# Optimization experiments

Measured on AMD Instinct MI355X. Metric: run time of the kernel, lower is better.

The kernel has to match this reference:

```python
import jax, jax.numpy as jnp
import numpy as np

N_NODES = 50000
N_EDGES = 800000
F_IN = 128
HEADS = 8
C = 16  # per-head channels (out_channels 128 // heads 8)
NEG_SLOPE = 0.2


def setup_inputs() -> dict:
    key = jax.random.key(0)
    k1, k2, k3, k4, k5, k6 = jax.random.split(key, 6)
    x = jax.random.normal(k1, (N_NODES, F_IN), dtype=jnp.float32)
    edge_index = jax.random.randint(k2, (2, N_EDGES), 0, N_NODES, dtype=jnp.int32)
    s = 1.0 / np.sqrt(F_IN)
    W_l = jax.random.normal(k3, (HEADS * C, F_IN), dtype=jnp.float32) * s
    W_r = jax.random.normal(k4, (HEADS * C, F_IN), dtype=jnp.float32) * s
    att = jax.random.normal(k5, (HEADS, C), dtype=jnp.float32) * s
    bias = jax.random.normal(k6, (HEADS * C,), dtype=jnp.float32) * 0.01
    return {"x": x, "edge_index": edge_index, "W_l": W_l, "W_r": W_r,
            "att": att, "bias": bias}


def reference(x, edge_index, W_l, W_r, att, bias):
    n = x.shape[0]
    src, dst = edge_index[0], edge_index[1]
    # node-level linear projections, reshaped to [n, H, C]
    x_l = (x @ W_l.T).reshape(n, HEADS, C)  # source features (x_j)
    x_r = (x @ W_r.T).reshape(n, HEADS, C)  # target features (x_i)
    x_j = x_l[src]          # [m, H, C] gathered per edge
    x_i = x_r[dst]          # [m, H, C]
    e = jax.nn.leaky_relu(x_i + x_j, NEG_SLOPE)      # [m, H, C]
    alpha = jnp.einsum('mhc,hc->mh', e, att)         # [m, H]
    # segment softmax over incoming edges of each target node (stable)
    amax = jax.ops.segment_max(alpha, dst, num_segments=n)   # [n, H]
    ea = jnp.exp(alpha - amax[dst])
    denom = jax.ops.segment_sum(ea, dst, num_segments=n)     # [n, H]
    alpha = ea / (denom[dst] + 1e-16)
    # scatter-aggregate messages x_j * alpha to target nodes
    out = jax.ops.segment_sum(x_j * alpha[..., None], dst, num_segments=n)
    out = out.reshape(n, HEADS * C) + bias  # concat heads + bias
    return out
```

## Files before the change

kernel.cpp:

```cpp
#include <hip/hip_runtime.h>
#include <hip/hip_fp16.h>
#include <math.h>


#define NN 50000
#define NE 800000
#define NHEADS 8
#define CH 16
#define FDIM 128
#define NEG_SLOPE 0.2f

#define BSHIFT 8
#define NBUCK ((NN + 255) >> 8)
#define BCAP 5120
#define CHUNK 4096
#define NCHUNK ((NE + CHUNK - 1) / CHUNK)

typedef _Float16 half8 __attribute__((ext_vector_type(8)));
typedef _Float16 h2v  __attribute__((ext_vector_type(2)));
typedef float f32x4 __attribute__((ext_vector_type(4)));

#define PBM 64
#define PTILES ((NN + PBM - 1) / PBM)

__global__ __launch_bounds__(512) void gat_proj_mfma(
        const float* __restrict__ x,
        const float* __restrict__ Wl,
        const float* __restrict__ Wr,
        __half* __restrict__ xl,
        __half* __restrict__ xr) {
    __shared__ __half Al[PBM][FDIM];
    __shared__ __half Bl[256][FDIM];

    const int t    = threadIdx.x;
    const int lane = t & 63;
    const int wave = t >> 6;
    const int wm   = wave >> 2;
    const int wn   = wave & 3;
    const int lr   = lane & 15;
    const int lh   = lane >> 4;

    const int row0 = blockIdx.x * PBM;

    #pragma unroll
    for (int i = 0; i < 2; ++i) {
        int c   = t + i * 512;
        int row = c >> 4;
        int c16 = c & 15;
        int sc  = c16 ^ (row & 7);
        int arow = row0 + row;
        if (arow >= NN) arow = NN - 1;
        const float4* src = reinterpret_cast<const float4*>(
            x + (size_t)arow * FDIM + c16 * 8);
        float4 v0 = src[0];
        float4 v1 = src[1];
        union { uint4 u; __half2 h[4]; } pk;
        pk.h[0] = __floats2half2_rn(v0.x, v0.y);
        pk.h[1] = __floats2half2_rn(v0.z, v0.w);
        pk.h[2] = __floats2half2_rn(v1.x, v1.y);
        pk.h[3] = __floats2half2_rn(v1.z, v1.w);
        *reinterpret_cast<uint4*>(&Al[row][sc * 8]) = pk.u;
    }
    #pragma unroll
    for (int i = 0; i < 8; ++i) {
        int c   = t + i * 512;
        int row = c >> 4;
        int c16 = c & 15;
        int sc  = c16 ^ (row & 7);
        const float* wr = (row < 128) ? (Wl + (size_t)row * FDIM)
                                      : (Wr + (size_t)(row - 128) * FDIM);
        const float4* src = reinterpret_cast<const float4*>(wr + c16 * 8);
        float4 v0 = src[0];
        float4 v1 = src[1];
        union { uint4 u; __half2 h[4]; } pk;
        pk.h[0] = __floats2half2_rn(v0.x, v0.y);
        pk.h[1] = __floats2half2_rn(v0.z, v0.w);
        pk.h[2] = __floats2half2_rn(v1.x, v1.y);
        pk.h[3] = __floats2half2_rn(v1.z, v1.w);
        *reinterpret_cast<uint4*>(&Bl[row][sc * 8]) = pk.u;
    }
    __syncthreads();

    f32x4 acc[2][4] = {};
    const char* Ab = reinterpret_cast<const char*>(&Al[0][0]);
    const char* Bb = reinterpret_cast<const char*>(&Bl[0][0]);

    #pragma unroll
    for (int kc = 0; kc < 4; ++kc) {
        half8 a[2], b[4];
        #pragma unroll
        for (int mi = 0; mi < 2; ++mi) {
            int row = wm * 32 + mi * 16 + lr;
            int bc  = (kc * 64 + 16 * lh) ^ ((row & 7) << 4);
            a[mi] = *reinterpret_cast<const half8*>(Ab + row * 256 + bc);
        }
        #pragma unroll
        for (int ni = 0; ni < 4; ++ni) {
            int row = wn * 64 + ni * 16 + lr;
            int bc  = (kc * 64 + 16 * lh) ^ ((row & 7) << 4);
            b[ni] = *reinterpret_cast<const half8*>(Bb + row * 256 + bc);
        }
        #pragma unroll
        for (int mi = 0; mi < 2; ++mi)
            #pragma unroll
            for (int ni = 0; ni < 4; ++ni)
                acc[mi][ni] = __builtin_amdgcn_mfma_f32_16x16x32_f16(
                    a[mi], b[ni], acc[mi][ni], 0, 0, 0);
    }

    #pragma unroll
    for (int mi = 0; mi < 2; ++mi) {
        #pragma unroll
        for (int ni = 0; ni < 4; ++ni) {
            int gc = wn * 64 + ni * 16 + lr;
            __half* outp = (gc < 128) ? xl : xr;
            int col = gc & 127;
            #pragma unroll
            for (int r = 0; r < 4; ++r) {
                int grow = row0 + wm * 32 + mi * 16 + 4 * lh + r;
                if (grow < NN)
                    outp[(size_t)grow * FDIM + col] = __float2half(acc[mi][ni][r]);
            }
        }
    }
}

__global__ void gat_init_cursor(int* __restrict__ bcursor) {
    int t = threadIdx.x;
    if (t < NBUCK) bcursor[t] = t * BCAP;
}

__global__ __launch_bounds__(256) void gat_bin_pass(
        const int* __restrict__ ei,
        int* __restrict__ bcursor,
        int2* __restrict__ binned) {
    __shared__ int hist[NBUCK];
    __shared__ int base_l[NBUCK];
    int t = threadIdx.x;
    for (int i = t; i < NBUCK; i += 256) hist[i] = 0;
    __syncthreads();

    int cbase = blockIdx.x * CHUNK;
    int s[CHUNK / 256], d[CHUNK / 256], r[CHUNK / 256];
    #pragma unroll
    for (int i = 0; i < CHUNK / 256; ++i) {
        int m = cbase + i * 256 + t;
        if (m < NE) {
            s[i] = ei[m];
            d[i] = ei[NE + m];
            r[i] = atomicAdd(&hist[d[i] >> BSHIFT], 1);
        } else {
            d[i] = -1;
        }
    }
    __syncthreads();
    for (int i = t; i < NBUCK; i += 256)
        base_l[i] = hist[i] ? atomicAdd(&bcursor[i], hist[i]) : 0;
    __syncthreads();
    #pragma unroll
    for (int i = 0; i < CHUNK / 256; ++i) {
        if (d[i] >= 0) {
            int pos = base_l[d[i] >> BSHIFT] + r[i];
            binned[pos] = make_int2(s[i], d[i] & 255);
        }
    }
}

__global__ __launch_bounds__(256) void gat_fine_pass(
        const int2* __restrict__ binned,
        const int* __restrict__ bcursor,
        int* __restrict__ rowstart,
        int* __restrict__ rowend,
        int* __restrict__ csr_src) {
    __shared__ int cnt_c[256];
    __shared__ int sbuf[256];
    __shared__ int cur_c[256];
    int t = threadIdx.x;
    int b = blockIdx.x;
    int base = b * BCAP;
    int cnt  = bcursor[b] - base;

    cnt_c[t] = 0;
    __syncthreads();
    for (int j = t; j < cnt; j += 256)
        atomicAdd(&cnt_c[binned[base + j].y], 1);
    __syncthreads();

    int v = cnt_c[t];
    sbuf[t] = v;
    __syncthreads();
    for (int off = 1; off < 256; off <<= 1) {
        int add = (t >= off) ? sbuf[t - off] : 0;
        __syncthreads();
        sbuf[t] += add;
        __syncthreads();
    }
    int excl = sbuf[t] - v;
    cur_c[t] = excl;
    int node = (b << BSHIFT) + t;
    if (node < NN) {
        rowstart[node] = base + excl;
        rowend[node]   = base + excl + v;
    }
    __syncthreads();

    for (int j = t; j < cnt; j += 256) {
        int2 e = binned[base + j];
        int pos = atomicAdd(&cur_c[e.y], 1);
        csr_src[base + pos] = e.x;
    }
}

__device__ __forceinline__ float gat_dot4_h(h2v e01, h2v e23,
                                            h2v at01, h2v at23) {
#if __has_builtin(__builtin_amdgcn_fdot2)
    float p = __builtin_amdgcn_fdot2(e01, at01, 0.0f, false);
    return __builtin_amdgcn_fdot2(e23, at23, p, false);
#else
    return (float)e01[0] * (float)at01[0] + (float)e01[1] * (float)at01[1]
         + (float)e23[0] * (float)at23[0] + (float)e23[1] * (float)at23[1];
#endif
}

__device__ __forceinline__ void gat_edge_step_h(
        const h2v xi01, const h2v xi23,
        const h2v at01, const h2v at23,
        uint2 raw, float4& acc, float& den) {
    union uh { unsigned u; h2v v; };
    uh j01, j23;
    j01.u = raw.x; j23.u = raw.y;
    h2v s01 = xi01 + j01.v;
    h2v s23 = xi23 + j23.v;
    uh b01, b23, a01, a23;
    b01.v = s01; b23.v = s23;
    a01.u = b01.u & 0x7FFF7FFFu;
    a23.u = b23.u & 0x7FFF7FFFu;
    const h2v c1 = {(_Float16)0.6f, (_Float16)0.6f};
    const h2v c2 = {(_Float16)0.4f, (_Float16)0.4f};
    h2v e01 = s01 * c1 + a01.v * c2;
    h2v e23 = s23 * c1 + a23.v * c2;
    float p = gat_dot4_h(e01, e23, at01, at23);
    p += __shfl_xor(p, 1);
    p += __shfl_xor(p, 2);
    float ea = __expf(p);
    acc.x = fmaf((float)j01.v[0], ea, acc.x);
    acc.y = fmaf((float)j01.v[1], ea, acc.y);
    acc.z = fmaf((float)j23.v[0], ea, acc.z);
    acc.w = fmaf((float)j23.v[1], ea, acc.w);
    den += ea;
}

__global__ __launch_bounds__(256) void gat_aggregate_kernel(
        const __half* __restrict__ xl,
        const __half* __restrict__ xr,
        const float* __restrict__ att,
        const float* __restrict__ bias,
        const int* __restrict__ rowstart,
        const int* __restrict__ rowend,
        const int* __restrict__ csr_src,
        float* __restrict__ out) {
    int node = blockIdx.x * 8 + (threadIdx.x >> 5);
    int u = threadIdx.x & 31;
    if (node >= NN) return;

    union { uint2 r; struct { unsigned a, b; } w; } xiraw;
    xiraw.r = *reinterpret_cast<const uint2*>(xr + (size_t)node * FDIM + u * 4);
    union uh { unsigned u; h2v v; };
    uh xi0, xi1;
    xi0.u = xiraw.w.a; xi1.u = xiraw.w.b;
    const float4 atf = *reinterpret_cast<const float4*>(att + u * 4);
    h2v a01 = {(_Float16)atf.x, (_Float16)atf.y};
    h2v a23 = {(_Float16)atf.z, (_Float16)atf.w};
    const float4 bi = *reinterpret_cast<const float4*>(bias + u * 4);
    int e0 = rowstart[node];
    int e1 = rowend[node];

    float4 acc0 = {0,0,0,0}, acc1 = {0,0,0,0}, acc2 = {0,0,0,0}, acc3 = {0,0,0,0};
    float den0 = 0.0f, den1 = 0.0f, den2 = 0.0f, den3 = 0.0f;

    int e = e0;
    for (; e + 4 <= e1; e += 4) {
        int s0 = csr_src[e + 0];
        int s1 = csr_src[e + 1];
        int s2 = csr_src[e + 2];
        int s3 = csr_src[e + 3];
        uint2 r0 = *reinterpret_cast<const uint2*>(xl + (size_t)s0 * FDIM + u * 4);
        uint2 r1 = *reinterpret_cast<const uint2*>(xl + (size_t)s1 * FDIM + u * 4);
        uint2 r2 = *reinterpret_cast<const uint2*>(xl + (size_t)s2 * FDIM + u * 4);
        uint2 r3 = *reinterpret_cast<const uint2*>(xl + (size_t)s3 * FDIM + u * 4);
        gat_edge_step_h(xi0.v, xi1.v, a01, a23, r0, acc0, den0);
        gat_edge_step_h(xi0.v, xi1.v, a01, a23, r1, acc1, den1);
        gat_edge_step_h(xi0.v, xi1.v, a01, a23, r2, acc2, den2);
        gat_edge_step_h(xi0.v, xi1.v, a01, a23, r3, acc3, den3);
    }
    for (; e < e1; ++e) {
        int s0 = csr_src[e];
        uint2 r0 = *reinterpret_cast<const uint2*>(xl + (size_t)s0 * FDIM + u * 4);
        gat_edge_step_h(xi0.v, xi1.v, a01, a23, r0, acc0, den0);
    }

    float4 acc;
    acc.x = (acc0.x + acc1.x) + (acc2.x + acc3.x);
    acc.y = (acc0.y + acc1.y) + (acc2.y + acc3.y);
    acc.z = (acc0.z + acc1.z) + (acc2.z + acc3.z);
    acc.w = (acc0.w + acc1.w) + (acc2.w + acc3.w);
    float den = (den0 + den1) + (den2 + den3);

    float inv = 1.0f / (den + 1e-16f);
    float4 o;
    o.x = acc.x * inv + bi.x;
    o.y = acc.y * inv + bi.y;
    o.z = acc.z * inv + bi.z;
    o.w = acc.w * inv + bi.w;
    *reinterpret_cast<float4*>(out + (size_t)node * FDIM + u * 4) = o;
}

extern "C" void kernel_launch(void* const* d_in, const int* in_sizes, int n_in,
                              void* d_out, int out_size, void* d_ws, size_t ws_size,
                              hipStream_t stream) {
    const float* x    = (const float*)d_in[0];
    const int*   ei   = (const int*)d_in[1];
    const float* Wl   = (const float*)d_in[2];
    const float* Wr   = (const float*)d_in[3];
    const float* att  = (const float*)d_in[4];
    const float* bias = (const float*)d_in[5];
    float* out = (float*)d_out;

    __half* xl = (__half*)d_ws;
    __half* xr = xl + (size_t)NN * FDIM;
    int2* binned   = (int2*)(xr + (size_t)NN * FDIM);
    int* csr_src   = (int*)(binned + (size_t)NBUCK * BCAP);
    int* rowstart  = csr_src + (size_t)NBUCK * BCAP;
    int* rowend    = rowstart + NN + 8;
    int* bcursor   = rowend + NN + 8;

    gat_init_cursor<<<1, 256, 0, stream>>>(bcursor);
    gat_bin_pass<<<NCHUNK, 256, 0, stream>>>(ei, bcursor, binned);
    gat_fine_pass<<<NBUCK, 256, 0, stream>>>(binned, bcursor, rowstart, rowend, csr_src);

    gat_proj_mfma<<<PTILES, 512, 0, stream>>>(x, Wl, Wr, xl, xr);

    gat_aggregate_kernel<<<(NN + 7) / 8, 256, 0, stream>>>(
        xl, xr, att, bias, rowstart, rowend, csr_src, out);
}
```

Before: 87.27 us.

## Pack binned edges into 32 bits, use 16-bit CSR indices, widen aggregate lanes

Binned edges are packed into a single 32-bit word (source shifted left by 8, local destination in the low 8 bits) instead of an int2. The fine pass stages them in shared memory so global memory is read only once. CSR source indices are stored as 16-bit values, which can represent every node index below 65536. The aggregate kernel now gives each node 16 lanes, each loading 8 halves with a 128-bit load, which cuts one shuffle step and doubles nodes per block, at the cost of more registers per thread.

Result: no change. 88.11 us (+1.0%).

```diff
diff --git a/kernel.cpp b/kernel.cpp
--- a/kernel.cpp
+++ b/kernel.cpp
@@ -133,7 +133,7 @@
 __global__ __launch_bounds__(256) void gat_bin_pass(
         const int* __restrict__ ei,
         int* __restrict__ bcursor,
-        int2* __restrict__ binned) {
+        unsigned* __restrict__ binned) {
     __shared__ int hist[NBUCK];
     __shared__ int base_l[NBUCK];
     int t = threadIdx.x;
@@ -161,17 +161,18 @@
     for (int i = 0; i < CHUNK / 256; ++i) {
         if (d[i] >= 0) {
             int pos = base_l[d[i] >> BSHIFT] + r[i];
-            binned[pos] = make_int2(s[i], d[i] & 255);
+            binned[pos] = ((unsigned)s[i] << 8) | (unsigned)(d[i] & 255);
         }
     }
 }
 
 __global__ __launch_bounds__(256) void gat_fine_pass(
-        const int2* __restrict__ binned,
+        const unsigned* __restrict__ binned,
         const int* __restrict__ bcursor,
         int* __restrict__ rowstart,
         int* __restrict__ rowend,
-        int* __restrict__ csr_src) {
+        unsigned short* __restrict__ csr16) {
+    __shared__ unsigned ebuf[BCAP];
     __shared__ int cnt_c[256];
     __shared__ int sbuf[256];
     __shared__ int cur_c[256];
@@ -180,10 +181,11 @@
     int base = b * BCAP;
     int cnt  = bcursor[b] - base;
 
+    for (int j = t; j < cnt; j += 256) ebuf[j] = binned[base + j];
     cnt_c[t] = 0;
     __syncthreads();
     for (int j = t; j < cnt; j += 256)
-        atomicAdd(&cnt_c[binned[base + j].y], 1);
+        atomicAdd(&cnt_c[ebuf[j] & 255u], 1);
     __syncthreads();
 
     int v = cnt_c[t];
@@ -205,48 +207,54 @@
     __syncthreads();
 
     for (int j = t; j < cnt; j += 256) {
-        int2 e = binned[base + j];
-        int pos = atomicAdd(&cur_c[e.y], 1);
-        csr_src[base + pos] = e.x;
-    }
-}
-
-__device__ __forceinline__ float gat_dot4_h(h2v e01, h2v e23,
-                                            h2v at01, h2v at23) {
+        unsigned e = ebuf[j];
+        int pos = atomicAdd(&cur_c[e & 255u], 1);
+        csr16[base + pos] = (unsigned short)(e >> 8);
+    }
+}
+
+__device__ __forceinline__ float gat_dot8_h(const h2v e[4], const h2v at[4]) {
 #if __has_builtin(__builtin_amdgcn_fdot2)
-    float p = __builtin_amdgcn_fdot2(e01, at01, 0.0f, false);
-    return __builtin_amdgcn_fdot2(e23, at23, p, false);
+    float p = __builtin_amdgcn_fdot2(e[0], at[0], 0.0f, false);
+    p = __builtin_amdgcn_fdot2(e[1], at[1], p, false);
+    p = __builtin_amdgcn_fdot2(e[2], at[2], p, false);
+    return __builtin_amdgcn_fdot2(e[3], at[3], p, false);
 #else
-    return (float)e01[0] * (float)at01[0] + (float)e01[1] * (float)at01[1]
-         + (float)e23[0] * (float)at23[0] + (float)e23[1] * (float)at23[1];
+    float p = 0.f;
+    for (int q = 0; q < 4; ++q)
+        p += (float)e[q][0] * (float)at[q][0] + (float)e[q][1] * (float)at[q][1];
+    return p;
 #endif
 }
 
-__device__ __forceinline__ void gat_edge_step_h(
-        const h2v xi01, const h2v xi23,
-        const h2v at01, const h2v at23,
-        uint2 raw, float4& acc, float& den) {
+__device__ __forceinline__ void gat_edge_step8(
+        const h2v xi[4], const h2v at[4], uint4 raw,
+        float4& accA, float4& accB, float& den) {
     union uh { unsigned u; h2v v; };
-    uh j01, j23;
-    j01.u = raw.x; j23.u = raw.y;
-    h2v s01 = xi01 + j01.v;
-    h2v s23 = xi23 + j23.v;
-    uh b01, b23, a01, a23;
-    b01.v = s01; b23.v = s23;
-    a01.u = b01.u & 0x7FFF7FFFu;
-    a23.u = b23.u & 0x7FFF7FFFu;
+    uh j[4];
+    j[0].u = raw.x; j[1].u = raw.y; j[2].u = raw.z; j[3].u = raw.w;
     const h2v c1 = {(_Float16)0.6f, (_Float16)0.6f};
     const h2v c2 = {(_Float16)0.4f, (_Float16)0.4f};
-    h2v e01 = s01 * c1 + a01.v * c2;
-    h2v e23 = s23 * c1 + a23.v * c2;
-    float p = gat_dot4_h(e01, e23, at01, at23);
+    h2v e[4];
+    #pragma unroll
+    for (int q = 0; q < 4; ++q) {
+        h2v s = xi[q] + j[q].v;
+        uh bb, aa;
+        bb.v = s;
+        aa.u = bb.u & 0x7FFF7FFFu;
+        e[q] = s * c1 + aa.v * c2;
+    }
+    float p = gat_dot8_h(e, at);
     p += __shfl_xor(p, 1);
-    p += __shfl_xor(p, 2);
     float ea = __expf(p);
-    acc.x = fmaf((float)j01.v[0], ea, acc.x);
-    acc.y = fmaf((float)j01.v[1], ea, acc.y);
-    acc.z = fmaf((float)j23.v[0], ea, acc.z);
-    acc.w = fmaf((float)j23.v[1], ea, acc.w);
+    accA.x = fmaf((float)j[0].v[0], ea, accA.x);
+    accA.y = fmaf((float)j[0].v[1], ea, accA.y);
+    accA.z = fmaf((float)j[1].v[0], ea, accA.z);
+    accA.w = fmaf((float)j[1].v[1], ea, accA.w);
+    accB.x = fmaf((float)j[2].v[0], ea, accB.x);
+    accB.y = fmaf((float)j[2].v[1], ea, accB.y);
+    accB.z = fmaf((float)j[3].v[0], ea, accB.z);
+    accB.w = fmaf((float)j[3].v[1], ea, accB.w);
     den += ea;
 }
 
@@ -257,62 +265,80 @@
         const float* __restrict__ bias,
         const int* __restrict__ rowstart,
         const int* __restrict__ rowend,
-        const int* __restrict__ csr_src,
+        const unsigned short* __restrict__ csr16,
         float* __restrict__ out) {
-    int node = blockIdx.x * 8 + (threadIdx.x >> 5);
-    int u = threadIdx.x & 31;
+    int node = blockIdx.x * 16 + (threadIdx.x >> 4);
+    int u = threadIdx.x & 15;
     if (node >= NN) return;
 
-    union { uint2 r; struct { unsigned a, b; } w; } xiraw;
-    xiraw.r = *reinterpret_cast<const uint2*>(xr + (size_t)node * FDIM + u * 4);
+    uint4 xiraw = *reinterpret_cast<const uint4*>(xr + (size_t)node * FDIM + u * 8);
     union uh { unsigned u; h2v v; };
-    uh xi0, xi1;
-    xi0.u = xiraw.w.a; xi1.u = xiraw.w.b;
-    const float4 atf = *reinterpret_cast<const float4*>(att + u * 4);
-    h2v a01 = {(_Float16)atf.x, (_Float16)atf.y};
-    h2v a23 = {(_Float16)atf.z, (_Float16)atf.w};
-    const float4 bi = *reinterpret_cast<const float4*>(bias + u * 4);
+    h2v xi[4];
+    { uh w; w.u = xiraw.x; xi[0] = w.v; w.u = xiraw.y; xi[1] = w.v;
+      w.u = xiraw.z; xi[2] = w.v; w.u = xiraw.w; xi[3] = w.v; }
+    const float4 atf0 = *reinterpret_cast<const float4*>(att + u * 8);
+    const float4 atf1 = *reinterpret_cast<const float4*>(att + u * 8 + 4);
+    h2v at[4];
+    at[0] = (h2v){(_Float16)atf0.x, (_Float16)atf0.y};
+    at[1] = (h2v){(_Float16)atf0.z, (_Float16)atf0.w};
+    at[2] = (h2v){(_Float16)atf1.x, (_Float16)atf1.y};
+    at[3] = (h2v){(_Float16)atf1.z, (_Float16)atf1.w};
+    const float4 bi0 = *reinterpret_cast<const float4*>(bias + u * 8);
+    const float4 bi1 = *reinterpret_cast<const float4*>(bias + u * 8 + 4);
     int e0 = rowstart[node];
     int e1 = rowend[node];
 
-    float4 acc0 = {0,0,0,0}, acc1 = {0,0,0,0}, acc2 = {0,0,0,0}, acc3 = {0,0,0,0};
-    float den0 = 0.0f, den1 = 0.0f, den2 = 0.0f, den3 = 0.0f;
+    float4 aA0 = {0,0,0,0}, aB0 = {0,0,0,0};
+    float4 aA1 = {0,0,0,0}, aB1 = {0,0,0,0};
+    float4 aA2 = {0,0,0,0}, aB2 = {0,0,0,0};
+    float4 aA3 = {0,0,0,0}, aB3 = {0,0,0,0};
+    float den0 = 0.f, den1 = 0.f, den2 = 0.f, den3 = 0.f;
 
     int e = e0;
     for (; e + 4 <= e1; e += 4) {
-        int s0 = csr_src[e + 0];
-        int s1 = csr_src[e + 1];
-        int s2 = csr_src[e + 2];
-        int s3 = csr_src[e + 3];
-        uint2 r0 = *reinterpret_cast<const uint2*>(xl + (size_t)s0 * FDIM + u * 4);
-        uint2 r1 = *reinterpret_cast<const uint2*>(xl + (size_t)s1 * FDIM + u * 4);
-        uint2 r2 = *reinterpret_cast<const uint2*>(xl + (size_t)s2 * FDIM + u * 4);
-        uint2 r3 = *reinterpret_cast<const uint2*>(xl + (size_t)s3 * FDIM + u * 4);
-        gat_edge_step_h(xi0.v, xi1.v, a01, a23, r0, acc0, den0);
-        gat_edge_step_h(xi0.v, xi1.v, a01, a23, r1, acc1, den1);
-        gat_edge_step_h(xi0.v, xi1.v, a01, a23, r2, acc2, den2);
-        gat_edge_step_h(xi0.v, xi1.v, a01, a23, r3, acc3, den3);
+        int s0 = csr16[e + 0];
+        int s1 = csr16[e + 1];
+        int s2 = csr16[e + 2];
+        int s3 = csr16[e + 3];
+        uint4 r0 = *reinterpret_cast<const uint4*>(xl + (size_t)s0 * FDIM + u * 8);
+        uint4 r1 = *reinterpret_cast<const uint4*>(xl + (size_t)s1 * FDIM + u * 8);
+        uint4 r2 = *reinterpret_cast<const uint4*>(xl + (size_t)s2 * FDIM + u * 8);
+        uint4 r3 = *reinterpret_cast<const uint4*>(xl + (size_t)s3 * FDIM + u * 8);
+        gat_edge_step8(xi, at, r0, aA0, aB0, den0);
+        gat_edge_step8(xi, at, r1, aA1, aB1, den1);
+        gat_edge_step8(xi, at, r2, aA2, aB2, den2);
+        gat_edge_step8(xi, at, r3, aA3, aB3, den3);
     }
     for (; e < e1; ++e) {
-        int s0 = csr_src[e];
-        uint2 r0 = *reinterpret_cast<const uint2*>(xl + (size_t)s0 * FDIM + u * 4);
-        gat_edge_step_h(xi0.v, xi1.v, a01, a23, r0, acc0, den0);
-    }
-
-    float4 acc;
-    acc.x = (acc0.x + acc1.x) + (acc2.x + acc3.x);
-    acc.y = (acc0.y + acc1.y) + (acc2.y + acc3.y);
-    acc.z = (acc0.z + acc1.z) + (acc2.z + acc3.z);
-    acc.w = (acc0.w + acc1.w) + (acc2.w + acc3.w);
+        int s0 = csr16[e];
+        uint4 r0 = *reinterpret_cast<const uint4*>(xl + (size_t)s0 * FDIM + u * 8);
+        gat_edge_step8(xi, at, r0, aA0, aB0, den0);
+    }
+
+    float4 accA, accB;
+    accA.x = (aA0.x + aA1.x) + (aA2.x + aA3.x);
+    accA.y = (aA0.y + aA1.y) + (aA2.y + aA3.y);
+    accA.z = (aA0.z + aA1.z) + (aA2.z + aA3.z);
+    accA.w = (aA0.w + aA1.w) + (aA2.w + aA3.w);
+    accB.x = (aB0.x + aB1.x) + (aB2.x + aB3.x);
+    accB.y = (aB0.y + aB1.y) + (aB2.y + aB3.y);
+    accB.z = (aB0.z + aB1.z) + (aB2.z + aB3.z);
+    accB.w = (aB0.w + aB1.w) + (aB2.w + aB3.w);
     float den = (den0 + den1) + (den2 + den3);
 
     float inv = 1.0f / (den + 1e-16f);
-    float4 o;
-    o.x = acc.x * inv + bi.x;
-    o.y = acc.y * inv + bi.y;
-    o.z = acc.z * inv + bi.z;
-    o.w = acc.w * inv + bi.w;
-    *reinterpret_cast<float4*>(out + (size_t)node * FDIM + u * 4) = o;
+    float4 o0, o1;
+    o0.x = accA.x * inv + bi0.x;
+    o0.y = accA.y * inv + bi0.y;
+    o0.z = accA.z * inv + bi0.z;
+    o0.w = accA.w * inv + bi0.w;
+    o1.x = accB.x * inv + bi1.x;
+    o1.y = accB.y * inv + bi1.y;
+    o1.z = accB.z * inv + bi1.z;
+    o1.w = accB.w * inv + bi1.w;
+    float* op = out + (size_t)node * FDIM + u * 8;
+    *reinterpret_cast<float4*>(op)     = o0;
+    *reinterpret_cast<float4*>(op + 4) = o1;
 }
 
 extern "C" void kernel_launch(void* const* d_in, const int* in_sizes, int n_in,
@@ -328,18 +354,18 @@
 
     __half* xl = (__half*)d_ws;
     __half* xr = xl + (size_t)NN * FDIM;
-    int2* binned   = (int2*)(xr + (size_t)NN * FDIM);
-    int* csr_src   = (int*)(binned + (size_t)NBUCK * BCAP);
-    int* rowstart  = csr_src + (size_t)NBUCK * BCAP;
+    unsigned* binned = (unsigned*)(xr + (size_t)NN * FDIM);
+    unsigned short* csr16 = (unsigned short*)(binned + (size_t)NBUCK * BCAP);
+    int* rowstart  = (int*)(csr16 + (size_t)NBUCK * BCAP);
     int* rowend    = rowstart + NN + 8;
     int* bcursor   = rowend + NN + 8;
 
     gat_init_cursor<<<1, 256, 0, stream>>>(bcursor);
     gat_bin_pass<<<NCHUNK, 256, 0, stream>>>(ei, bcursor, binned);
-    gat_fine_pass<<<NBUCK, 256, 0, stream>>>(binned, bcursor, rowstart, rowend, csr_src);
+    gat_fine_pass<<<NBUCK, 256, 0, stream>>>(binned, bcursor, rowstart, rowend, csr16);
 
     gat_proj_mfma<<<PTILES, 512, 0, stream>>>(x, Wl, Wr, xl, xr);
 
-    gat_aggregate_kernel<<<(NN + 7) / 8, 256, 0, stream>>>(
-        xl, xr, att, bias, rowstart, rowend, csr_src, out);
-}
+    gat_aggregate_kernel<<<(NN + 15) / 16, 256, 0, stream>>>(
+        xl, xr, att, bias, rowstart, rowend, csr16, out);
+}
```

## Pack binned edges into 32-bit words, use 16-bit CSR sources, exp2 scoring

Applied to the files above, without the earlier changes.

Each binned edge is packed into one 32-bit word (source shifted left by 8, local destination in the low byte) and the CSR source array is stored as 16-bit indices. This roughly halves the bytes moved by the binning and CSR passes and the index loads in aggregation. The fine pass stages each bucket in shared memory so the binned array is read once instead of twice. The aggregation folds log2(e) into the attention vector so it can use exp2f, and it collapses the four partial accumulators into one. That single accumulator frees registers but lengthens the dependency chain, and the 16-bit indices rely on the node count fitting in 16 bits.

Measured after the change: 83.85 us. -3.9%, faster.

```diff
diff --git a/kernel.cpp b/kernel.cpp
--- a/kernel.cpp
+++ b/kernel.cpp
@@ -9,6 +9,7 @@
 #define CH 16
 #define FDIM 128
 #define NEG_SLOPE 0.2f
+#define LOG2E 1.44269504088896f
 
 #define BSHIFT 8
 #define NBUCK ((NN + 255) >> 8)
@@ -133,7 +134,7 @@
 __global__ __launch_bounds__(256) void gat_bin_pass(
         const int* __restrict__ ei,
         int* __restrict__ bcursor,
-        int2* __restrict__ binned) {
+        unsigned* __restrict__ binned) {
     __shared__ int hist[NBUCK];
     __shared__ int base_l[NBUCK];
     int t = threadIdx.x;
@@ -161,17 +162,18 @@
     for (int i = 0; i < CHUNK / 256; ++i) {
         if (d[i] >= 0) {
             int pos = base_l[d[i] >> BSHIFT] + r[i];
-            binned[pos] = make_int2(s[i], d[i] & 255);
+            binned[pos] = ((unsigned)s[i] << 8) | (unsigned)(d[i] & 255);
         }
     }
 }
 
 __global__ __launch_bounds__(256) void gat_fine_pass(
-        const int2* __restrict__ binned,
+        const unsigned* __restrict__ binned,
         const int* __restrict__ bcursor,
         int* __restrict__ rowstart,
         int* __restrict__ rowend,
-        int* __restrict__ csr_src) {
+        unsigned short* __restrict__ csr16) {
+    __shared__ unsigned ebuf[BCAP];
     __shared__ int cnt_c[256];
     __shared__ int sbuf[256];
     __shared__ int cur_c[256];
@@ -180,10 +182,11 @@
     int base = b * BCAP;
     int cnt  = bcursor[b] - base;
 
+    for (int j = t; j < cnt; j += 256) ebuf[j] = binned[base + j];
     cnt_c[t] = 0;
     __syncthreads();
     for (int j = t; j < cnt; j += 256)
-        atomicAdd(&cnt_c[binned[base + j].y], 1);
+        atomicAdd(&cnt_c[ebuf[j] & 255u], 1);
     __syncthreads();
 
     int v = cnt_c[t];
@@ -205,21 +208,10 @@
     __syncthreads();
 
     for (int j = t; j < cnt; j += 256) {
-        int2 e = binned[base + j];
-        int pos = atomicAdd(&cur_c[e.y], 1);
-        csr_src[base + pos] = e.x;
-    }
-}
-
-__device__ __forceinline__ float gat_dot4_h(h2v e01, h2v e23,
-                                            h2v at01, h2v at23) {
-#if __has_builtin(__builtin_amdgcn_fdot2)
-    float p = __builtin_amdgcn_fdot2(e01, at01, 0.0f, false);
-    return __builtin_amdgcn_fdot2(e23, at23, p, false);
-#else
-    return (float)e01[0] * (float)at01[0] + (float)e01[1] * (float)at01[1]
-         + (float)e23[0] * (float)at23[0] + (float)e23[1] * (float)at23[1];
-#endif
+        unsigned e = ebuf[j];
+        int pos = atomicAdd(&cur_c[e & 255u], 1);
+        csr16[base + pos] = (unsigned short)(e >> 8);
+    }
 }
 
 __device__ __forceinline__ void gat_edge_step_h(
@@ -239,10 +231,16 @@
     const h2v c2 = {(_Float16)0.4f, (_Float16)0.4f};
     h2v e01 = s01 * c1 + a01.v * c2;
     h2v e23 = s23 * c1 + a23.v * c2;
-    float p = gat_dot4_h(e01, e23, at01, at23);
+#if __has_builtin(__builtin_amdgcn_fdot2)
+    float p = __builtin_amdgcn_fdot2(e01, at01, 0.0f, false);
+    p = __builtin_amdgcn_fdot2(e23, at23, p, false);
+#else
+    float p = (float)e01[0] * (float)at01[0] + (float)e01[1] * (float)at01[1]
+            + (float)e23[0] * (float)at23[0] + (float)e23[1] * (float)at23[1];
+#endif
     p += __shfl_xor(p, 1);
     p += __shfl_xor(p, 2);
-    float ea = __expf(p);
+    float ea = exp2f(p);
     acc.x = fmaf((float)j01.v[0], ea, acc.x);
     acc.y = fmaf((float)j01.v[1], ea, acc.y);
     acc.z = fmaf((float)j23.v[0], ea, acc.z);
@@ -257,54 +255,46 @@
         const float* __restrict__ bias,
         const int* __restrict__ rowstart,
         const int* __restrict__ rowend,
-        const int* __restrict__ csr_src,
+        const unsigned short* __restrict__ csr16,
         float* __restrict__ out) {
     int node = blockIdx.x * 8 + (threadIdx.x >> 5);
     int u = threadIdx.x & 31;
     if (node >= NN) return;
 
-    union { uint2 r; struct { unsigned a, b; } w; } xiraw;
-    xiraw.r = *reinterpret_cast<const uint2*>(xr + (size_t)node * FDIM + u * 4);
     union uh { unsigned u; h2v v; };
+    uint2 xiraw = *reinterpret_cast<const uint2*>(xr + (size_t)node * FDIM + u * 4);
     uh xi0, xi1;
-    xi0.u = xiraw.w.a; xi1.u = xiraw.w.b;
+    xi0.u = xiraw.x; xi1.u = xiraw.y;
     const float4 atf = *reinterpret_cast<const float4*>(att + u * 4);
-    h2v a01 = {(_Float16)atf.x, (_Float16)atf.y};
-    h2v a23 = {(_Float16)atf.z, (_Float16)atf.w};
+    h2v a01 = {(_Float16)(atf.x * LOG2E), (_Float16)(atf.y * LOG2E)};
+    h2v a23 = {(_Float16)(atf.z * LOG2E), (_Float16)(atf.w * LOG2E)};
     const float4 bi = *reinterpret_cast<const float4*>(bias + u * 4);
     int e0 = rowstart[node];
     int e1 = rowend[node];
 
-    float4 acc0 = {0,0,0,0}, acc1 = {0,0,0,0}, acc2 = {0,0,0,0}, acc3 = {0,0,0,0};
-    float den0 = 0.0f, den1 = 0.0f, den2 = 0.0f, den3 = 0.0f;
+    float4 acc = {0, 0, 0, 0};
+    float den = 0.0f;
 
     int e = e0;
     for (; e + 4 <= e1; e += 4) {
-        int s0 = csr_src[e + 0];
-        int s1 = csr_src[e + 1];
-        int s2 = csr_src[e + 2];
-        int s3 = csr_src[e + 3];
+        int s0 = csr16[e + 0];
+        int s1 = csr16[e + 1];
+        int s2 = csr16[e + 2];
+        int s3 = csr16[e + 3];
         uint2 r0 = *reinterpret_cast<const uint2*>(xl + (size_t)s0 * FDIM + u * 4);
         uint2 r1 = *reinterpret_cast<const uint2*>(xl + (size_t)s1 * FDIM + u * 4);
         uint2 r2 = *reinterpret_cast<const uint2*>(xl + (size_t)s2 * FDIM + u * 4);
         uint2 r3 = *reinterpret_cast<const uint2*>(xl + (size_t)s3 * FDIM + u * 4);
-        gat_edge_step_h(xi0.v, xi1.v, a01, a23, r0, acc0, den0);
-        gat_edge_step_h(xi0.v, xi1.v, a01, a23, r1, acc1, den1);
-        gat_edge_step_h(xi0.v, xi1.v, a01, a23, r2, acc2, den2);
-        gat_edge_step_h(xi0.v, xi1.v, a01, a23, r3, acc3, den3);
+        gat_edge_step_h(xi0.v, xi1.v, a01, a23, r0, acc, den);
+        gat_edge_step_h(xi0.v, xi1.v, a01, a23, r1, acc, den);
+        gat_edge_step_h(xi0.v, xi1.v, a01, a23, r2, acc, den);
+        gat_edge_step_h(xi0.v, xi1.v, a01, a23, r3, acc, den);
     }
     for (; e < e1; ++e) {
-        int s0 = csr_src[e];
+        int s0 = csr16[e];
         uint2 r0 = *reinterpret_cast<const uint2*>(xl + (size_t)s0 * FDIM + u * 4);
-        gat_edge_step_h(xi0.v, xi1.v, a01, a23, r0, acc0, den0);
-    }
-
-    float4 acc;
-    acc.x = (acc0.x + acc1.x) + (acc2.x + acc3.x);
-    acc.y = (acc0.y + acc1.y) + (acc2.y + acc3.y);
-    acc.z = (acc0.z + acc1.z) + (acc2.z + acc3.z);
-    acc.w = (acc0.w + acc1.w) + (acc2.w + acc3.w);
-    float den = (den0 + den1) + (den2 + den3);
+        gat_edge_step_h(xi0.v, xi1.v, a01, a23, r0, acc, den);
+    }
 
     float inv = 1.0f / (den + 1e-16f);
     float4 o;
@@ -328,18 +318,18 @@
 
     __half* xl = (__half*)d_ws;
     __half* xr = xl + (size_t)NN * FDIM;
-    int2* binned   = (int2*)(xr + (size_t)NN * FDIM);
-    int* csr_src   = (int*)(binned + (size_t)NBUCK * BCAP);
-    int* rowstart  = csr_src + (size_t)NBUCK * BCAP;
+    unsigned* binned = (unsigned*)(xr + (size_t)NN * FDIM);
+    unsigned short* csr16 = (unsigned short*)(binned + (size_t)NBUCK * BCAP);
+    int* rowstart  = (int*)(csr16 + (size_t)NBUCK * BCAP);
     int* rowend    = rowstart + NN + 8;
     int* bcursor   = rowend + NN + 8;
 
     gat_init_cursor<<<1, 256, 0, stream>>>(bcursor);
     gat_bin_pass<<<NCHUNK, 256, 0, stream>>>(ei, bcursor, binned);
-    gat_fine_pass<<<NBUCK, 256, 0, stream>>>(binned, bcursor, rowstart, rowend, csr_src);
+    gat_fine_pass<<<NBUCK, 256, 0, stream>>>(binned, bcursor, rowstart, rowend, csr16);
 
     gat_proj_mfma<<<PTILES, 512, 0, stream>>>(x, Wl, Wr, xl, xr);
 
     gat_aggregate_kernel<<<(NN + 7) / 8, 256, 0, stream>>>(
-        xl, xr, att, bias, rowstart, rowend, csr_src, out);
-}
+        xl, xr, att, bias, rowstart, rowend, csr16, out);
+}
```
